# Kernel tuning notes

Hardware: AMD Instinct MI355X
Metric: run time of the kernel (lower is better)

## Reference

```python
import jax, jax.numpy as jnp
import numpy as np

# Episode configuration (matches init_kwargs); feature map fixed by module: [64,7,7]
N_WAY, K_SHOT, Q_QUERY, PRJ = 10, 5, 100, 16
DIM, H, W = 64, 7, 7
N_SUP = N_WAY * K_SHOT * PRJ      # 800 support samples
N_QRY = N_WAY * Q_QUERY * PRJ     # 16000 query samples
B = N_SUP + N_QRY                 # 16800
TRIU_I, TRIU_J = np.triu_indices(DIM)  # row-major upper-tri indices, matches torch nonzero order


def setup_inputs() -> dict:
    key = jax.random.key(0)
    k1, k2 = jax.random.split(key)
    feat = jax.random.normal(k1, (B, DIM, H, W), dtype=jnp.float32)
    label = jax.random.randint(k2, (N_QRY,), 0, N_WAY, dtype=jnp.int64)
    # nn.Parameter init: log(1/(2*h*w)) * ones(1,1)
    temp = jnp.log(jnp.ones((1, 1), dtype=jnp.float32) / (2.0 * H * W))
    return {"feat": feat, "temp": temp, "label": label}


def _bdcovpool(x, t):
    # x: [B, dim, h, w] -> Brownian distance covariance matrix [B, dim, dim]
    b, d, h, w = x.shape
    xm = x.reshape(b, d, h * w)
    g = jnp.einsum('bim,bjm->bij', xm, xm)            # x @ x^T, [B,d,d]
    dg = jnp.diagonal(g, axis1=1, axis2=2)            # [B,d]
    # I_M @ (G*I) + (G*I) @ I_M - 2G  ==  diag_j + diag_i - 2G
    dcov = dg[:, None, :] + dg[:, :, None] - 2.0 * g
    dcov = jnp.sqrt(jnp.exp(t) * jnp.clip(dcov, 0.0) + 1e-5)
    # double centering: dcov - rowmean - colmean + totalmean
    rm = jnp.mean(dcov, axis=2, keepdims=True)        # (1/d) dcov @ I_M
    cm = jnp.mean(dcov, axis=1, keepdims=True)        # (1/d) I_M @ dcov
    tm = jnp.mean(dcov, axis=(1, 2), keepdims=True)   # (1/d^2) I_M @ dcov @ I_M
    return dcov - rm - cm + tm


def reference(feat, temp, label):
    v = _bdcovpool(feat, temp)                        # [B, 64, 64]
    tv = v[:, TRIU_I, TRIU_J]                         # Triuvec: [B, 2080]
    support = tv[:N_SUP].reshape(N_WAY, K_SHOT * PRJ, -1).mean(axis=1)  # [n_way, 2080]
    query = tv[N_SUP:]                                # [N_QRY, 2080]
    # negative squared euclidean distance (expanded form of sum((x-y)^2))
    q2 = jnp.sum(query * query, axis=1, keepdims=True)          # [N_QRY,1]
    s2 = jnp.sum(support * support, axis=1)[None, :]             # [1,n_way]
    score = -(q2 + s2 - 2.0 * jnp.einsum('nd,md->nm', query, support))  # [N_QRY, n_way]
    logp = jax.nn.log_softmax(score, axis=-1)
    loss = -jnp.mean(jnp.take_along_axis(logp, label[:, None], axis=1))
    return score, loss
```

## Files before the change

kernel.cpp:

```cpp
#include <hip/hip_runtime.h>
#include <math.h>

#define NWAY   10
#define DIMD   64
#define HWN    49
#define NSUP   800
#define NQRY   16000
#define NTRI   2080
#define FEAT_PER (DIMD*HWN)
#define LDST   68
#define KPAD   72

typedef __attribute__((ext_vector_type(8))) short bf16x8;
typedef __attribute__((ext_vector_type(4))) float f32x4;

struct __align__(16) BDCShared {
    union {
        float dcov[DIMD*LDST];
        unsigned short hl[2*DIMD*KPAD];
    } u;
    float dg[DIMD];
    float rm[DIMD];
    float psum[4*DIMD];
    float red[4*12];
    float tm;
};

__device__ __forceinline__ void k2ij(int k, int& io, int& jo) {
    int ii = (int)floorf((129.0f - sqrtf(16641.0f - 8.0f*(float)k)) * 0.5f);
    int off = ii*(129-ii)/2;
    if (off > k) { --ii; off = ii*(129-ii)/2; }
    else {
        int off2 = (ii+1)*(128-ii)/2;
        if (off2 <= k) { ii += 1; off = off2; }
    }
    io = ii;
    jo = ii + (k - off);
}

__device__ __forceinline__ unsigned short f32_to_bf16_rn(float x) {
    unsigned u = __float_as_uint(x);
    return (unsigned short)((u + 0x7fffu + ((u >> 16) & 1u)) >> 16);
}

__device__ __forceinline__ float bdc_compute(const float* __restrict__ feat,
                                             float et, int sample,
                                             BDCShared& sm) {
    const int tid = threadIdx.x;
    unsigned short* H = sm.u.hl;
    unsigned short* Lp = sm.u.hl + DIMD*KPAD;

    const float4* f4 = (const float4*)(feat + (size_t)sample * FEAT_PER);
    for (int idx = tid; idx < FEAT_PER/4; idx += 256) {
        float4 v = f4[idx];
        int e = idx * 4;
        #pragma unroll
        for (int kk = 0; kk < 4; ++kk) {
            int el = e + kk;
            int d = el / HWN;
            int m = el - d * HWN;
            float x = (&v.x)[kk];
            unsigned short hu = f32_to_bf16_rn(x);
            float hf = __uint_as_float(((unsigned)hu) << 16);
            unsigned short lu = f32_to_bf16_rn(x - hf);
            H[d*KPAD + m]  = hu;
            Lp[d*KPAD + m] = lu;
        }
    }
    for (int p = tid; p < DIMD*16; p += 256) {
        int d = p >> 4, k = 48 + (p & 15);
        if (k >= HWN) { H[d*KPAD + k] = 0; Lp[d*KPAD + k] = 0; }
    }
    __syncthreads();

    const int wv = tid >> 6, lane = tid & 63;
    const int qd = lane >> 4, c15 = lane & 15;
    const int abase = (16*wv + c15)*KPAD + qd*8;
    bf16x8 AH0 = *(const bf16x8*)&H[abase];
    bf16x8 AH1 = *(const bf16x8*)&H[abase + 32];
    bf16x8 AL0 = *(const bf16x8*)&Lp[abase];
    bf16x8 AL1 = *(const bf16x8*)&Lp[abase + 32];

    f32x4 acc[4];
    #pragma unroll
    for (int J = 0; J < 4; ++J) {
        const int bbase = (16*J + c15)*KPAD + qd*8;
        bf16x8 BH0 = *(const bf16x8*)&H[bbase];
        bf16x8 BH1 = *(const bf16x8*)&H[bbase + 32];
        bf16x8 BL0 = *(const bf16x8*)&Lp[bbase];
        bf16x8 BL1 = *(const bf16x8*)&Lp[bbase + 32];
        f32x4 a = {0.f, 0.f, 0.f, 0.f};
        a = __builtin_amdgcn_mfma_f32_16x16x32_bf16(AH0, BH0, a, 0, 0, 0);
        a = __builtin_amdgcn_mfma_f32_16x16x32_bf16(AH1, BH1, a, 0, 0, 0);
        a = __builtin_amdgcn_mfma_f32_16x16x32_bf16(AL0, BH0, a, 0, 0, 0);
        a = __builtin_amdgcn_mfma_f32_16x16x32_bf16(AL1, BH1, a, 0, 0, 0);
        a = __builtin_amdgcn_mfma_f32_16x16x32_bf16(AH0, BL0, a, 0, 0, 0);
        a = __builtin_amdgcn_mfma_f32_16x16x32_bf16(AH1, BL1, a, 0, 0, 0);
        acc[J] = a;
    }

    #pragma unroll
    for (int J = 0; J < 4; ++J) {
        if (J == wv) {
            #pragma unroll
            for (int r = 0; r < 4; ++r)
                if (c15 == 4*qd + r) sm.dg[16*wv + c15] = acc[J][r];
        }
    }
    __syncthreads();

    float* dcov = sm.u.dcov;
    float dgi[4];
    #pragma unroll
    for (int r = 0; r < 4; ++r) dgi[r] = sm.dg[16*wv + 4*qd + r];
    #pragma unroll
    for (int J = 0; J < 4; ++J) {
        int j = 16*J + c15;
        float dgj = sm.dg[j];
        #pragma unroll
        for (int r = 0; r < 4; ++r) {
            int i = 16*wv + 4*qd + r;
            float val = dgi[r] + dgj - 2.0f*acc[J][r];
            dcov[i*LDST + j] = sqrtf(et * fmaxf(val, 0.0f) + 1e-5f);
        }
    }
    __syncthreads();

    {
        int c = tid & 63, q = tid >> 6;
        float s = 0.0f;
        #pragma unroll
        for (int i2 = 0; i2 < 16; ++i2) s += dcov[(q*16 + i2)*LDST + c];
        sm.psum[q*DIMD + c] = s;
    }
    __syncthreads();
    if (tid < DIMD) {
        sm.rm[tid] = (sm.psum[tid] + sm.psum[DIMD+tid] +
                      sm.psum[2*DIMD+tid] + sm.psum[3*DIMD+tid]) * (1.0f/64.0f);
    }
    __syncthreads();
    if (tid < DIMD) {
        float v = sm.rm[tid];
        #pragma unroll
        for (int o = 32; o > 0; o >>= 1) v += __shfl_xor(v, o, 64);
        if (tid == 0) sm.tm = v * (1.0f/64.0f);
    }
    __syncthreads();
    return sm.tm;
}

__global__ void kern_init(float* __restrict__ support,
                          unsigned* __restrict__ table,
                          float* __restrict__ loss_slot) {
    int i = blockIdx.x * 256 + threadIdx.x;
    if (i < NWAY*NTRI) support[i] = 0.0f;
    if (i < NTRI) {
        int ii, jj; k2ij(i, ii, jj);
        table[i] = ((unsigned)(ii*LDST + jj) << 16) | ((unsigned)ii << 8) | (unsigned)jj;
    }
    if (i == 0) loss_slot[0] = 0.0f;
}

__global__ __launch_bounds__(256, 6) void kern_support(const float* __restrict__ feat,
                                                       const float* __restrict__ temp,
                                                       const unsigned* __restrict__ table,
                                                       float* __restrict__ support) {
    __shared__ BDCShared sm;
    float et = __expf(temp[0]);
    int s = blockIdx.x;
    float tm = bdc_compute(feat, et, s, sm);
    float* dst = support + (s / 80) * NTRI;
    for (int k = threadIdx.x; k < NTRI; k += 256) {
        unsigned t = table[k];
        float v = sm.u.dcov[t >> 16] - sm.rm[(t >> 8) & 63] - sm.rm[t & 63] + tm;
        atomicAdd(&dst[k], v * (1.0f/80.0f));
    }
}

__global__ __launch_bounds__(256) void kern_s2(const float* __restrict__ support,
                                               float* __restrict__ s2) {
    __shared__ float red[4];
    int m = blockIdx.x;
    const float* S = support + m * NTRI;
    float acc = 0.0f;
    for (int k = threadIdx.x; k < NTRI; k += 256) acc = fmaf(S[k], S[k], acc);
    int lane = threadIdx.x & 63, wv = threadIdx.x >> 6;
    #pragma unroll
    for (int o = 32; o > 0; o >>= 1) acc += __shfl_xor(acc, o, 64);
    if (lane == 0) red[wv] = acc;
    __syncthreads();
    if (threadIdx.x == 0) s2[m] = red[0] + red[1] + red[2] + red[3];
}

__global__ __launch_bounds__(256, 6) void kern_query(const float* __restrict__ feat,
                                                     const float* __restrict__ temp,
                                                     const unsigned* __restrict__ table,
                                                     const float* __restrict__ support,
                                                     const float* __restrict__ s2,
                                                     float* __restrict__ out) {
    __shared__ BDCShared sm;
    float et = __expf(temp[0]);
    int qn = blockIdx.x;
    float tm = bdc_compute(feat, et, NSUP + qn, sm);

    float qq = 0.0f;
    float cr[NWAY];
    #pragma unroll
    for (int m = 0; m < NWAY; ++m) cr[m] = 0.0f;

    for (int k = threadIdx.x; k < NTRI; k += 256) {
        unsigned t = table[k];
        float v = sm.u.dcov[t >> 16] - sm.rm[(t >> 8) & 63] - sm.rm[t & 63] + tm;
        qq = fmaf(v, v, qq);
        #pragma unroll
        for (int m = 0; m < NWAY; ++m)
            cr[m] = fmaf(v, support[m*NTRI + k], cr[m]);
    }

    int lane = threadIdx.x & 63, wv = threadIdx.x >> 6;
    #pragma unroll
    for (int m = 0; m < NWAY; ++m) {
        float v = cr[m];
        #pragma unroll
        for (int o = 32; o > 0; o >>= 1) v += __shfl_xor(v, o, 64);
        cr[m] = v;
    }
    #pragma unroll
    for (int o = 32; o > 0; o >>= 1) qq += __shfl_xor(qq, o, 64);
    if (lane == 0) {
        #pragma unroll
        for (int m = 0; m < NWAY; ++m) sm.red[wv*12 + m] = cr[m];
        sm.red[wv*12 + 10] = qq;
    }
    __syncthreads();
    if (threadIdx.x < NWAY) {
        int m = threadIdx.x;
        float CR = sm.red[m] + sm.red[12+m] + sm.red[24+m] + sm.red[36+m];
        float QQ = sm.red[10] + sm.red[22] + sm.red[34] + sm.red[46];
        out[(size_t)qn * NWAY + m] = -(QQ + s2[m] - 2.0f*CR);
    }
}

__global__ __launch_bounds__(256) void kern_loss(const float* __restrict__ score,
                                                 const int* __restrict__ label,
                                                 float* __restrict__ loss_out) {
    __shared__ float red[4];
    int n = blockIdx.x * 256 + threadIdx.x;
    float lsum = 0.0f;
    if (n < NQRY) {
        const float* srow = score + (size_t)n * NWAY;
        float s[NWAY];
        float mx = -1e30f;
        #pragma unroll
        for (int m = 0; m < NWAY; ++m) { s[m] = srow[m]; mx = fmaxf(mx, s[m]); }
        float se = 0.0f;
        #pragma unroll
        for (int m = 0; m < NWAY; ++m) se += __expf(s[m] - mx);
        float lse = mx + __logf(se);
        lsum = lse - s[label[n]];
    }
    int lane = threadIdx.x & 63, wv = threadIdx.x >> 6;
    #pragma unroll
    for (int o = 32; o > 0; o >>= 1) lsum += __shfl_xor(lsum, o, 64);
    if (lane == 0) red[wv] = lsum;
    __syncthreads();
    if (threadIdx.x == 0)
        atomicAdd(loss_out, (red[0] + red[1] + red[2] + red[3]) * (1.0f / (float)NQRY));
}

extern "C" void kernel_launch(void* const* d_in, const int* in_sizes, int n_in,
                              void* d_out, int out_size, void* d_ws, size_t ws_size,
                              hipStream_t stream) {
    const float* feat = (const float*)d_in[0];
    const float* temp = (const float*)d_in[1];
    const int*   label = (const int*)d_in[2];
    float* out = (float*)d_out;

    float*    support = (float*)d_ws;
    float*    s2      = support + NWAY*NTRI;
    unsigned* table   = (unsigned*)(s2 + 16);
    float* loss_slot  = out + (size_t)NQRY * NWAY;

    kern_init<<<(NWAY*NTRI + 255)/256, 256, 0, stream>>>(support, table, loss_slot);
    kern_support<<<NSUP, 256, 0, stream>>>(feat, temp, table, support);
    kern_s2<<<NWAY, 256, 0, stream>>>(support, s2);
    kern_query<<<NQRY, 256, 0, stream>>>(feat, temp, table, support, s2, out);
    kern_loss<<<(NQRY + 255)/256, 256, 0, stream>>>(out, label, loss_slot);
}
```

Baseline: 385.7 us.

## Fold centering constants and compute query norm algebraically from dcov sums

The bf16 hi/lo split now truncates instead of round-to-nearest. The total mean is folded into a centered row-mean vector, which removes one barrier and the tm broadcast. The query's squared norm over the upper triangle is now derived in closed form from the sum of squared dcov entries and the row means, using a constant for the diagonal value. That constant only holds when the diagonal of dcov equals sqrt(1e-5). The triangle loops are fully unrolled with fixed strides. This cuts per-element ALU work and the reduction in the query loop, at some risk of numerical differences from the truncating split and the closed-form norm.

```diff
diff --git a/kernel.cpp b/kernel.cpp
--- a/kernel.cpp
+++ b/kernel.cpp
@@ -10,6 +10,7 @@
 #define FEAT_PER (DIMD*HWN)
 #define LDST   68
 #define KPAD   72
+#define S0DIAG 3.16227766e-3f
 
 typedef __attribute__((ext_vector_type(8))) short bf16x8;
 typedef __attribute__((ext_vector_type(4))) float f32x4;
@@ -20,10 +21,11 @@
         unsigned short hl[2*DIMD*KPAD];
     } u;
     float dg[DIMD];
-    float rm[DIMD];
+    float rmc[DIMD];
     float psum[4*DIMD];
-    float red[4*12];
-    float tm;
+    float red[4*NWAY];
+    float red2[4];
+    float qq;
 };
 
 __device__ __forceinline__ void k2ij(int k, int& io, int& jo) {
@@ -38,14 +40,9 @@
     jo = ii + (k - off);
 }
 
-__device__ __forceinline__ unsigned short f32_to_bf16_rn(float x) {
-    unsigned u = __float_as_uint(x);
-    return (unsigned short)((u + 0x7fffu + ((u >> 16) & 1u)) >> 16);
-}
-
-__device__ __forceinline__ float bdc_compute(const float* __restrict__ feat,
-                                             float et, int sample,
-                                             BDCShared& sm) {
+__device__ __forceinline__ void bdc_compute(const float* __restrict__ feat,
+                                            float et, int sample,
+                                            BDCShared& sm) {
     const int tid = threadIdx.x;
     unsigned short* H = sm.u.hl;
     unsigned short* Lp = sm.u.hl + DIMD*KPAD;
@@ -60,11 +57,10 @@
             int d = el / HWN;
             int m = el - d * HWN;
             float x = (&v.x)[kk];
-            unsigned short hu = f32_to_bf16_rn(x);
-            float hf = __uint_as_float(((unsigned)hu) << 16);
-            unsigned short lu = f32_to_bf16_rn(x - hf);
-            H[d*KPAD + m]  = hu;
-            Lp[d*KPAD + m] = lu;
+            unsigned u = __float_as_uint(x);
+            float l = x - __uint_as_float(u & 0xffff0000u);
+            H[d*KPAD + m]  = (unsigned short)(u >> 16);
+            Lp[d*KPAD + m] = (unsigned short)(__float_as_uint(l) >> 16);
         }
     }
     for (int p = tid; p < DIMD*16; p += 256) {
@@ -117,36 +113,58 @@
     for (int J = 0; J < 4; ++J) {
         int j = 16*J + c15;
         float dgj = sm.dg[j];
+        float4 w;
         #pragma unroll
         for (int r = 0; r < 4; ++r) {
-            int i = 16*wv + 4*qd + r;
             float val = dgi[r] + dgj - 2.0f*acc[J][r];
-            dcov[i*LDST + j] = sqrtf(et * fmaxf(val, 0.0f) + 1e-5f);
-        }
+            (&w.x)[r] = __builtin_amdgcn_sqrtf(fmaf(et, fmaxf(val, 0.0f), 1e-5f));
+        }
+        #pragma unroll
+        for (int r = 0; r < 4; ++r)
+            dcov[(16*wv + 4*qd + r)*LDST + j] = (&w.x)[r];
     }
     __syncthreads();
 
     {
         int c = tid & 63, q = tid >> 6;
-        float s = 0.0f;
-        #pragma unroll
-        for (int i2 = 0; i2 < 16; ++i2) s += dcov[(q*16 + i2)*LDST + c];
+        float s = 0.0f, sq = 0.0f;
+        #pragma unroll
+        for (int i2 = 0; i2 < 16; ++i2) {
+            float d = dcov[(q*16 + i2)*LDST + c];
+            s += d;
+            sq = fmaf(d, d, sq);
+        }
         sm.psum[q*DIMD + c] = s;
+        #pragma unroll
+        for (int o = 32; o > 0; o >>= 1) sq += __shfl_xor(sq, o, 64);
+        if ((tid & 63) == 0) sm.red2[q] = sq;
     }
     __syncthreads();
     if (tid < DIMD) {
-        sm.rm[tid] = (sm.psum[tid] + sm.psum[DIMD+tid] +
-                      sm.psum[2*DIMD+tid] + sm.psum[3*DIMD+tid]) * (1.0f/64.0f);
-    }
-    __syncthreads();
-    if (tid < DIMD) {
-        float v = sm.rm[tid];
-        #pragma unroll
-        for (int o = 32; o > 0; o >>= 1) v += __shfl_xor(v, o, 64);
-        if (tid == 0) sm.tm = v * (1.0f/64.0f);
-    }
-    __syncthreads();
-    return sm.tm;
+        int i = tid;
+        float colsum = sm.psum[i] + sm.psum[DIMD+i] +
+                       sm.psum[2*DIMD+i] + sm.psum[3*DIMD+i];
+        float a = colsum * (1.0f/64.0f);
+        float sa = a;
+        #pragma unroll
+        for (int o = 32; o > 0; o >>= 1) sa += __shfl_xor(sa, o, 64);
+        float t = sa * (1.0f/64.0f);
+        float rmc = a - 0.5f*t;
+        sm.rmc[i] = rmc;
+        float ci = S0DIAG - 2.0f*rmc;
+        float p  = a*a;
+        float dd = ci*ci;
+        #pragma unroll
+        for (int o = 32; o > 0; o >>= 1) {
+            p  += __shfl_xor(p,  o, 64);
+            dd += __shfl_xor(dd, o, 64);
+        }
+        if (tid == 0) {
+            float sumd2 = sm.red2[0] + sm.red2[1] + sm.red2[2] + sm.red2[3];
+            sm.qq = 0.5f*((sumd2 - 128.0f*p) + (4096.0f*t*t + dd));
+        }
+    }
+    __syncthreads();
 }
 
 __global__ void kern_init(float* __restrict__ support,
@@ -168,12 +186,20 @@
     __shared__ BDCShared sm;
     float et = __expf(temp[0]);
     int s = blockIdx.x;
-    float tm = bdc_compute(feat, et, s, sm);
-    float* dst = support + (s / 80) * NTRI;
-    for (int k = threadIdx.x; k < NTRI; k += 256) {
-        unsigned t = table[k];
-        float v = sm.u.dcov[t >> 16] - sm.rm[(t >> 8) & 63] - sm.rm[t & 63] + tm;
-        atomicAdd(&dst[k], v * (1.0f/80.0f));
+    bdc_compute(feat, et, s, sm);
+    const int tid = threadIdx.x;
+    float* dst = support + (s / 80) * NTRI + tid;
+    const unsigned* tb = table + tid;
+    #pragma unroll
+    for (int u = 0; u < 8; ++u) {
+        unsigned t = tb[256*u];
+        float v = sm.u.dcov[t >> 16] - sm.rmc[(t >> 8) & 63] - sm.rmc[t & 63];
+        atomicAdd(&dst[256*u], v * (1.0f/80.0f));
+    }
+    if (tid < 32) {
+        unsigned t = tb[2048];
+        float v = sm.u.dcov[t >> 16] - sm.rmc[(t >> 8) & 63] - sm.rmc[t & 63];
+        atomicAdd(&dst[2048], v * (1.0f/80.0f));
     }
 }
 
@@ -201,23 +227,32 @@
     __shared__ BDCShared sm;
     float et = __expf(temp[0]);
     int qn = blockIdx.x;
-    float tm = bdc_compute(feat, et, NSUP + qn, sm);
-
-    float qq = 0.0f;
+    bdc_compute(feat, et, NSUP + qn, sm);
+    const int tid = threadIdx.x;
+
     float cr[NWAY];
     #pragma unroll
     for (int m = 0; m < NWAY; ++m) cr[m] = 0.0f;
 
-    for (int k = threadIdx.x; k < NTRI; k += 256) {
-        unsigned t = table[k];
-        float v = sm.u.dcov[t >> 16] - sm.rm[(t >> 8) & 63] - sm.rm[t & 63] + tm;
-        qq = fmaf(v, v, qq);
+    const unsigned* tb = table + tid;
+    const float* sp = support + tid;
+    #pragma unroll
+    for (int u = 0; u < 8; ++u) {
+        unsigned t = tb[256*u];
+        float v = sm.u.dcov[t >> 16] - sm.rmc[(t >> 8) & 63] - sm.rmc[t & 63];
         #pragma unroll
         for (int m = 0; m < NWAY; ++m)
-            cr[m] = fmaf(v, support[m*NTRI + k], cr[m]);
-    }
-
-    int lane = threadIdx.x & 63, wv = threadIdx.x >> 6;
+            cr[m] = fmaf(v, sp[m*NTRI + 256*u], cr[m]);
+    }
+    if (tid < 32) {
+        unsigned t = tb[2048];
+        float v = sm.u.dcov[t >> 16] - sm.rmc[(t >> 8) & 63] - sm.rmc[t & 63];
+        #pragma unroll
+        for (int m = 0; m < NWAY; ++m)
+            cr[m] = fmaf(v, sp[m*NTRI + 2048], cr[m]);
+    }
+
+    int lane = tid & 63, wv = tid >> 6;
     #pragma unroll
     for (int m = 0; m < NWAY; ++m) {
         float v = cr[m];
@@ -225,19 +260,15 @@
         for (int o = 32; o > 0; o >>= 1) v += __shfl_xor(v, o, 64);
         cr[m] = v;
     }
-    #pragma unroll
-    for (int o = 32; o > 0; o >>= 1) qq += __shfl_xor(qq, o, 64);
     if (lane == 0) {
         #pragma unroll
-        for (int m = 0; m < NWAY; ++m) sm.red[wv*12 + m] = cr[m];
-        sm.red[wv*12 + 10] = qq;
-    }
-    __syncthreads();
-    if (threadIdx.x < NWAY) {
-        int m = threadIdx.x;
-        float CR = sm.red[m] + sm.red[12+m] + sm.red[24+m] + sm.red[36+m];
-        float QQ = sm.red[10] + sm.red[22] + sm.red[34] + sm.red[46];
-        out[(size_t)qn * NWAY + m] = -(QQ + s2[m] - 2.0f*CR);
+        for (int m = 0; m < NWAY; ++m) sm.red[wv*NWAY + m] = cr[m];
+    }
+    __syncthreads();
+    if (tid < NWAY) {
+        int m = tid;
+        float CR = sm.red[m] + sm.red[NWAY+m] + sm.red[2*NWAY+m] + sm.red[3*NWAY+m];
+        out[(size_t)qn * NWAY + m] = -(sm.qq + s2[m] - 2.0f*CR);
     }
 }
 
```

Result: slower. 405.3 us (+5.1%).
